# Performance work log

Measured on AMD Instinct MI355X. Metric: run time of the kernel, lower is better.

The kernel has to match this reference:

```python
import jax, jax.numpy as jnp
import numpy as np

B, Cin, H, W = 1024, 384, 14, 14
C = 768        # out_dim of stage (embed_dim[-1])
HEADS = 24
WIN = 7        # window clamped to post-merge resolution (7x7), shift=0
HID = 512      # cpb_mlp hidden width (timm SwinV2 default)
MLP = 4 * C


def _rel_tables(win):
    # log-spaced continuous relative coords table [ (2w-1)^2, 2 ]
    rng = np.arange(-(win - 1), win, dtype=np.float32)
    t = np.stack(np.meshgrid(rng, rng, indexing='ij'), axis=-1)
    t = t / (win - 1) * 8.0  # pretrained_window_size == 0 branch
    t = np.sign(t) * np.log2(np.abs(t) + 1.0) / np.log2(8.0)
    coords = np.stack(np.meshgrid(np.arange(win), np.arange(win), indexing='ij'))
    cf = coords.reshape(2, -1)
    rel = (cf[:, :, None] - cf[:, None, :]).transpose(1, 2, 0).astype(np.int64)
    rel[:, :, 0] += win - 1
    rel[:, :, 1] += win - 1
    rel[:, :, 0] *= 2 * win - 1
    idx = rel.sum(-1)
    return jnp.asarray(t.reshape(-1, 2)), jnp.asarray(idx.reshape(-1))


def _ln(x, g, b, eps=1e-5):
    mu = jnp.mean(x, axis=-1, keepdims=True)
    var = jnp.mean(jnp.square(x - mu), axis=-1, keepdims=True)
    return (x - mu) * jax.lax.rsqrt(var + eps) * g + b


def setup_inputs() -> dict:
    key = jax.random.key(0)
    ks = jax.random.split(key, 8)
    s = 0.02
    return dict(
        x=jax.random.normal(ks[0], (B, Cin, H, W), jnp.float32),
        merge_w=jax.random.normal(ks[1], (C, 4 * Cin), jnp.float32) * s,
        merge_gamma=jnp.ones((C,), jnp.float32),
        merge_beta=jnp.zeros((C,), jnp.float32),
        qkv_w=jax.random.normal(ks[2], (2, 3 * C, C), jnp.float32) * s,
        q_bias=jnp.zeros((2, C), jnp.float32),
        v_bias=jnp.zeros((2, C), jnp.float32),
        logit_scale=jnp.full((2, HEADS, 1, 1), float(np.log(10.0)), jnp.float32),
        cpb_w1=jax.random.normal(ks[3], (2, HID, 2), jnp.float32) * s,
        cpb_b1=jnp.zeros((2, HID), jnp.float32),
        cpb_w2=jax.random.normal(ks[4], (2, HEADS, HID), jnp.float32) * s,
        proj_w=jax.random.normal(ks[5], (2, C, C), jnp.float32) * s,
        proj_b=jnp.zeros((2, C), jnp.float32),
        n1_g=jnp.ones((2, C), jnp.float32),
        n1_b=jnp.zeros((2, C), jnp.float32),
        fc1_w=jax.random.normal(ks[6], (2, MLP, C), jnp.float32) * s,
        fc1_b=jnp.zeros((2, MLP), jnp.float32),
        fc2_w=jax.random.normal(ks[7], (2, C, MLP), jnp.float32) * s,
        fc2_b=jnp.zeros((2, C), jnp.float32),
        n2_g=jnp.ones((2, C), jnp.float32),
        n2_b=jnp.zeros((2, C), jnp.float32),
    )


def reference(x, merge_w, merge_gamma, merge_beta, qkv_w, q_bias, v_bias,
              logit_scale, cpb_w1, cpb_b1, cpb_w2, proj_w, proj_b, n1_g, n1_b,
              fc1_w, fc1_b, fc2_w, fc2_b, n2_g, n2_b):
    table, idx = _rel_tables(WIN)
    hd = C // HEADS
    N = WIN * WIN
    # NCHW -> NHWC
    h = jnp.transpose(x, (0, 2, 3, 1))
    Bn = h.shape[0]
    # PatchMerging (SwinV2: reduction then norm)
    h = h.reshape(Bn, H // 2, 2, W // 2, 2, Cin).transpose(0, 1, 3, 4, 2, 5)
    h = h.reshape(Bn, H // 2, W // 2, 4 * Cin)
    h = h @ merge_w.T
    h = _ln(h, merge_gamma, merge_beta)
    h = h.reshape(Bn, N, C)  # single 7x7 window per ROI, shift=0
    max_ls = jnp.log(jnp.asarray(100.0, h.dtype))  # clamp logit_scale at log(1/0.01)
    for i in range(2):  # two structurally-identical blocks (post-norm)
        bias_qkv = jnp.concatenate([q_bias[i], jnp.zeros_like(q_bias[i]), v_bias[i]])
        qkv = (h @ qkv_w[i].T + bias_qkv).reshape(Bn, N, 3, HEADS, hd)
        q, k, v = jnp.moveaxis(qkv, 2, 0)  # each [B, N, HEADS, hd]
        q = q / jnp.maximum(jnp.linalg.norm(q, axis=-1, keepdims=True), 1e-12)
        k = k / jnp.maximum(jnp.linalg.norm(k, axis=-1, keepdims=True), 1e-12)
        attn = jnp.einsum('bnhd,bmhd->bhnm', q, k)
        attn = attn * jnp.exp(jnp.minimum(logit_scale[i], max_ls))  # [HEADS,1,1]
        # continuous relative position bias
        cpb = jax.nn.relu(table @ cpb_w1[i].T + cpb_b1[i]) @ cpb_w2[i].T  # [(2w-1)^2, HEADS]
        rpb = cpb[idx].reshape(N, N, HEADS).transpose(2, 0, 1)
        attn = attn + 16.0 * jax.nn.sigmoid(rpb)
        attn = jax.nn.softmax(attn, axis=-1)
        out = jnp.einsum('bhnm,bmhd->bnhd', attn, v).reshape(Bn, N, C)
        out = out @ proj_w[i].T + proj_b[i]
        h = h + _ln(out, n1_g[i], n1_b[i])  # post-norm residual
        m = jax.nn.gelu(h @ fc1_w[i].T + fc1_b[i], approximate=False)
        m = m @ fc2_w[i].T + fc2_b[i]
        h = h + _ln(m, n2_g[i], n2_b[i])
    h = h.reshape(Bn, WIN, WIN, C)
    return jnp.transpose(h, (0, 3, 1, 2))  # NHWC -> NCHW
```

## Files before the change

### kernel.cpp

```cpp
#include <hip/hip_runtime.h>

typedef unsigned short u16;
typedef unsigned int u32;
typedef __bf16 bf16x8 __attribute__((ext_vector_type(8)));
typedef float f32x4 __attribute__((ext_vector_type(4)));

#define AS1 __attribute__((address_space(1)))
#define AS3 __attribute__((address_space(3)))

__device__ __forceinline__ float b2f(u16 u) {
    u32 x = ((u32)u) << 16; float f; __builtin_memcpy(&f, &x, 4); return f;
}
__device__ __forceinline__ u16 f2b(float f) {
    u32 x; __builtin_memcpy(&x, &f, 4);
    x += 0x7fffu + ((x >> 16) & 1u);
    return (u16)(x >> 16);
}
__device__ __forceinline__ void gload16(void* s, const void* g) {
    __builtin_amdgcn_global_load_lds((const AS1 void*)g, (AS3 void*)s, 16, 0, 0);
}

__global__ void detect_kernel(const u32* __restrict__ mg, u32* __restrict__ flag) {
    if (threadIdx.x == 0) *flag = (mg[0] == 0x3F803F80u) ? 1u : 0u;
}

struct CvtW { const void* src[5]; long off[5]; int n[5]; };
__global__ __launch_bounds__(256) void cvt_w_kernel(CvtW J, u16* __restrict__ wbase,
                                                    const u32* __restrict__ flag) {
    const int tId = blockIdx.y;
    const long i0 = (long)blockIdx.x * 2048 + threadIdx.x * 8;
    if (i0 >= J.n[tId]) return;
    u16* dst = wbase + J.off[tId] + i0;
    if (*flag) {
        *(uint4*)dst = *((const uint4*)((const u16*)J.src[tId] + i0));
    } else {
        const float* s = (const float*)J.src[tId] + i0;
        u32 w[4];
#pragma unroll
        for (int k = 0; k < 4; k++)
            w[k] = (u32)f2b(s[2 * k]) | ((u32)f2b(s[2 * k + 1]) << 16);
        *(uint4*)dst = make_uint4(w[0], w[1], w[2], w[3]);
    }
}

struct CvtP { const void* src[15]; long off[15]; int n[15]; };
__global__ __launch_bounds__(256) void cvt_p_kernel(CvtP J, float* __restrict__ pbase,
                                                    const u32* __restrict__ flag) {
    const int tId = blockIdx.y;
    const long i0 = (long)blockIdx.x * 2048 + threadIdx.x * 8;
    if (i0 >= J.n[tId]) return;
    float* dst = pbase + J.off[tId] + i0;
    if (*flag) {
        const u16* s = (const u16*)J.src[tId] + i0;
#pragma unroll
        for (int k = 0; k < 8; k++) dst[k] = b2f(s[k]);
    } else {
        const float* s = (const float*)J.src[tId] + i0;
        *(float4*)dst = *(const float4*)s;
        *(float4*)(dst + 4) = *(const float4*)(s + 4);
    }
}

__global__ __launch_bounds__(256) void gather_merge(const void* __restrict__ xv,
                                                    u16* __restrict__ Am,
                                                    const u32* __restrict__ flag) {
    __shared__ __align__(16) char sraw[64 * 196 * 4];
    const int b = blockIdx.x, cc = blockIdx.y;
    const int t = threadIdx.x;
    const int isbf = *flag;
    if (isbf) {
        const u16* xp = (const u16*)xv + ((long)b * 384 + cc * 64) * 196;
        for (int i = t; i < 1568; i += 256)
            ((uint4*)sraw)[i] = ((const uint4*)xp)[i];
    } else {
        const float* xp = (const float*)xv + ((long)b * 384 + cc * 64) * 196;
        for (int i = t; i < 3136; i += 256)
            ((uint4*)sraw)[i] = ((const uint4*)xp)[i];
    }
    __syncthreads();
    const int c = t & 63, q = t >> 6;
    for (int sg = q; sg < 196; sg += 4) {
        const int sidx = sg >> 2, g = sg & 3;
        const int h2 = sidx / 7, w2 = sidx % 7, hi = g & 1, wi = g >> 1;
        const int hw = (2 * h2 + hi) * 14 + (2 * w2 + wi);
        const u16 val = isbf ? ((const u16*)sraw)[c * 196 + hw]
                             : f2b(((const float*)sraw)[c * 196 + hw]);
        Am[((long)b * 49 + sidx) * 1536 + g * 384 + cc * 64 + c] = val;
    }
}

template <int EPI>
__global__ __launch_bounds__(256) void gemm_bt(const u16* __restrict__ A,
                                               const u16* __restrict__ W,
                                               const float* __restrict__ bias,
                                               u16* __restrict__ D,
                                               int M, int N, int K) {
    __shared__ __align__(16) u16 sA[128 * 32];
    __shared__ __align__(16) u16 sB[128 * 32];
    const int t = threadIdx.x;
    const int lane = t & 63;
    const int wave = t >> 6;
    const long rowA0 = (long)blockIdx.y * 128;
    const long rowB0 = (long)blockIdx.x * 128;
    const int wm = (wave >> 1) * 64;
    const int wn = (wave & 1) * 64;

    f32x4 acc[4][4];
#pragma unroll
    for (int i = 0; i < 4; i++)
#pragma unroll
        for (int j = 0; j < 4; j++) acc[i][j] = (f32x4){0.f, 0.f, 0.f, 0.f};

    const int srow = t >> 2;
    const int scol = (t & 3) * 8;
    const int fr = lane & 15;
    const int fk = (lane >> 4) * 8;

    const u16* Ag = A + rowA0 * K;
    const u16* Bg = W + rowB0 * K;
    char* sAb = (char*)sA;
    char* sBb = (char*)sB;
    const int wb = wave * 1024;

    for (int kk = 0; kk < K; kk += 32) {
        gload16(sAb + wb,        Ag + (long)srow * K + kk + scol);
        gload16(sAb + 4096 + wb, Ag + (long)(64 + srow) * K + kk + scol);
        gload16(sBb + wb,        Bg + (long)srow * K + kk + scol);
        gload16(sBb + 4096 + wb, Bg + (long)(64 + srow) * K + kk + scol);
        __syncthreads();
        bf16x8 af[4], bf[4];
#pragma unroll
        for (int mt = 0; mt < 4; mt++)
            af[mt] = *(const bf16x8*)&sA[(wm + mt * 16 + fr) * 32 + fk];
#pragma unroll
        for (int nt = 0; nt < 4; nt++)
            bf[nt] = *(const bf16x8*)&sB[(wn + nt * 16 + fr) * 32 + fk];
#pragma unroll
        for (int mt = 0; mt < 4; mt++)
#pragma unroll
            for (int nt = 0; nt < 4; nt++)
                acc[mt][nt] = __builtin_amdgcn_mfma_f32_16x16x32_bf16(
                    af[mt], bf[nt], acc[mt][nt], 0, 0, 0);
        __syncthreads();
    }

#pragma unroll
    for (int mt = 0; mt < 4; mt++) {
#pragma unroll
        for (int nt = 0; nt < 4; nt++) {
            const long col = rowB0 + wn + nt * 16 + (lane & 15);
            const float bv = bias ? bias[col] : 0.f;
#pragma unroll
            for (int r = 0; r < 4; r++) {
                const long row = rowA0 + wm + mt * 16 + (lane >> 4) * 4 + r;
                float v = acc[mt][nt][r] + bv;
                if (EPI == 1) v = 0.5f * v * (1.f + erff(v * 0.70710678118654752f));
                D[row * N + col] = f2b(v);
            }
        }
    }
}

__global__ __launch_bounds__(256) void ln_kernel(const u16* __restrict__ y,
                                                 const float* __restrict__ gw,
                                                 const float* __restrict__ bw,
                                                 float* __restrict__ h32,
                                                 u16* __restrict__ hb, int add) {
    const int row = blockIdx.x * 4 + (threadIdx.x >> 6);
    const int lane = threadIdx.x & 63;
    const u16* yr = y + (long)row * 768;
    float v[12];
    float s = 0.f, s2 = 0.f;
#pragma unroll
    for (int c = 0; c < 3; c++) {
        uint2 u = *(const uint2*)(yr + c * 256 + lane * 4);
        u16 p[4]; __builtin_memcpy(p, &u, 8);
#pragma unroll
        for (int e = 0; e < 4; e++) {
            float f = b2f(p[e]); v[c * 4 + e] = f; s += f; s2 += f * f;
        }
    }
#pragma unroll
    for (int off = 32; off > 0; off >>= 1) {
        s += __shfl_down(s, off); s2 += __shfl_down(s2, off);
    }
    s = __shfl(s, 0); s2 = __shfl(s2, 0);
    const float mu = s * (1.f / 768.f);
    const float var = s2 * (1.f / 768.f) - mu * mu;
    const float rs = rsqrtf(fmaxf(var, 0.f) + 1e-5f);
#pragma unroll
    for (int c = 0; c < 3; c++) {
        const int idx = c * 256 + lane * 4;
        const float4 g4 = *(const float4*)(gw + idx);
        const float4 b4 = *(const float4*)(bw + idx);
        float o[4];
        o[0] = (v[c * 4 + 0] - mu) * rs * g4.x + b4.x;
        o[1] = (v[c * 4 + 1] - mu) * rs * g4.y + b4.y;
        o[2] = (v[c * 4 + 2] - mu) * rs * g4.z + b4.z;
        o[3] = (v[c * 4 + 3] - mu) * rs * g4.w + b4.w;
        const long gi = (long)row * 768 + idx;
        if (add) {
            float4 h4 = *(float4*)&h32[gi];
            o[0] += h4.x; o[1] += h4.y; o[2] += h4.z; o[3] += h4.w;
        }
        *(float4*)&h32[gi] = make_float4(o[0], o[1], o[2], o[3]);
        uint2 pk;
        pk.x = (u32)f2b(o[0]) | ((u32)f2b(o[1]) << 16);
        pk.y = (u32)f2b(o[2]) | ((u32)f2b(o[3]) << 16);
        *(uint2*)&hb[gi] = pk;
    }
}

__device__ __forceinline__ float reltab(int i) {
    float r = (float)(i - 6) * (8.f / 6.f);
    float a = fabsf(r);
    return copysignf(log2f(a + 1.f) * (1.f / 3.f), r);
}
__global__ __launch_bounds__(256) void cpb_kernel(const float* __restrict__ w1,
                                                  const float* __restrict__ b1,
                                                  const float* __restrict__ w2,
                                                  float* __restrict__ cpb) {
    __shared__ float hid[512];
    const int e = blockIdx.x;
    const float t0 = reltab(e / 13), t1 = reltab(e % 13);
    for (int k = threadIdx.x; k < 512; k += 256)
        hid[k] = fmaxf(w1[2 * k] * t0 + w1[2 * k + 1] * t1 + b1[k], 0.f);
    __syncthreads();
    const int wave = threadIdx.x >> 6, lane = threadIdx.x & 63;
    for (int h = wave; h < 24; h += 4) {
        float sum = 0.f;
        for (int k = lane; k < 512; k += 64) sum += w2[h * 512 + k] * hid[k];
#pragma unroll
        for (int off = 32; off > 0; off >>= 1) sum += __shfl_down(sum, off);
        if (lane == 0) cpb[e * 24 + h] = sum;
    }
}

__global__ void bias16_kernel(const float* __restrict__ cpb,
                              float* __restrict__ b16) {
    const int tid = blockIdx.x * 256 + threadIdx.x;
    if (tid >= 24 * 2401) return;
    const int h = tid / 2401, nm = tid % 2401;
    const int n = nm / 49, m = nm % 49;
    const int e = (n / 7 - m / 7 + 6) * 13 + (n % 7 - m % 7 + 6);
    b16[tid] = 16.f / (1.f + expf(-cpb[e * 24 + h]));
}

__global__ void qkvbias_kernel(const float* __restrict__ qb,
                               const float* __restrict__ vb,
                               float* __restrict__ out) {
    const int j = blockIdx.x * 256 + threadIdx.x;
    if (j >= 2304) return;
    float v = 0.f;
    if (j < 768) v = qb[j];
    else if (j >= 1536) v = vb[j - 1536];
    out[j] = v;
}

#define APAIRS 4
__global__ __launch_bounds__(256) void attn_kernel(const u16* __restrict__ qkv,
                                                   const float* __restrict__ b16,
                                                   const float* __restrict__ ls,
                                                   u16* __restrict__ out) {
    __shared__ float sk[APAIRS][49 * 33 + 3];
    __shared__ float sv[APAIRS][49 * 32];
    __shared__ float rk[APAIRS][52];
    const int wave = threadIdx.x >> 6;
    const int lane = threadIdx.x & 63;
    const int head = blockIdx.x;
    const int b = blockIdx.y * APAIRS + wave;
    const long base = (long)b * 49 * 2304 + head * 32;
    float* skw = sk[wave];
    float* svw = sv[wave];

    for (int qi = lane; qi < 392; qi += 64) {
        const int m = qi >> 3, d0 = (qi & 7) * 4;
        const long r = base + (long)m * 2304 + d0;
        uint2 kk = *(const uint2*)(qkv + r + 768);
        uint2 vv = *(const uint2*)(qkv + r + 1536);
        u16 kp[4], vp[4];
        __builtin_memcpy(kp, &kk, 8);
        __builtin_memcpy(vp, &vv, 8);
        const int ko = m * 33 + d0;
        const int vo = m * 32 + d0;
#pragma unroll
        for (int e = 0; e < 4; e++) {
            skw[ko + e] = b2f(kp[e]);
            svw[vo + e] = b2f(vp[e]);
        }
    }
    __syncthreads();
    const int n = lane;
    if (n < 49) {
        float ss = 0.f;
#pragma unroll
        for (int d = 0; d < 32; d++) { float kv = skw[n * 33 + d]; ss += kv * kv; }
        rk[wave][n] = 1.f / fmaxf(sqrtf(ss), 1e-12f);
    }
    __syncthreads();
    if (n >= 49) return;

    float q[32]; float ss = 0.f;
    {
        const u16* qp = qkv + base + (long)n * 2304;
#pragma unroll
        for (int c = 0; c < 4; c++) {
            uint4 u = *(const uint4*)(qp + c * 8);
            u16 p[8]; __builtin_memcpy(p, &u, 16);
#pragma unroll
            for (int e = 0; e < 8; e++) {
                float f = b2f(p[e]); q[c * 8 + e] = f; ss += f * f;
            }
        }
    }
    const float rq = 1.f / fmaxf(sqrtf(ss), 1e-12f);
    const float cs = expf(fminf(ls[head], 4.6051701859880914f)) * rq;
    const float* bb = b16 + head * 2401 + n * 49;
    const float* rkw = rk[wave];
    float sarr[49], mx = -1e30f;
#pragma unroll
    for (int m = 0; m < 49; m++) {
        float dot = 0.f;
#pragma unroll
        for (int d = 0; d < 32; d++) dot += q[d] * skw[m * 33 + d];
        float val = dot * cs * rkw[m] + bb[m];
        sarr[m] = val; mx = fmaxf(mx, val);
    }
    float sum = 0.f;
#pragma unroll
    for (int m = 0; m < 49; m++) { sarr[m] = __expf(sarr[m] - mx); sum += sarr[m]; }
    const float rsum = 1.f / sum;
    float o[32];
#pragma unroll
    for (int d = 0; d < 32; d++) o[d] = 0.f;
#pragma unroll
    for (int m = 0; m < 49; m++) {
        const float p = sarr[m];
        const float* vr = svw + m * 32;
#pragma unroll
        for (int d = 0; d < 32; d++) o[d] += p * vr[d];
    }
    u16* op = out + ((long)b * 49 + n) * 768 + head * 32;
#pragma unroll
    for (int d = 0; d < 32; d += 2) {
        u32 pk = (u32)f2b(o[d] * rsum) | ((u32)f2b(o[d + 1] * rsum) << 16);
        *(u32*)&op[d] = pk;
    }
}

__global__ __launch_bounds__(256) void out_transpose(const float* __restrict__ h32,
                                                     void* __restrict__ outv,
                                                     const u32* __restrict__ flag) {
    __shared__ __align__(16) float sbuf[49 * 196];
    const int b = blockIdx.x, cc = blockIdx.y;
    const float* hp = h32 + (long)b * 49 * 768 + cc * 192;
    for (int i = threadIdx.x; i < 49 * 48; i += 256) {
        const int r = i / 48, v = i % 48;
        *(float4*)&sbuf[r * 196 + v * 4] = *(const float4*)&hp[(long)r * 768 + v * 4];
    }
    __syncthreads();
    const int isbf = *flag;
    if (isbf) {
        u16* out = (u16*)outv;
        for (int i = threadIdx.x; i < 192 * 49; i += 256) {
            const int c = i / 49, s = i % 49;
            out[((long)b * 768 + cc * 192 + c) * 49 + s] = f2b(sbuf[s * 196 + c]);
        }
    } else {
        float* out = (float*)outv;
        for (int i = threadIdx.x; i < 192 * 49; i += 256) {
            const int c = i / 49, s = i % 49;
            out[((long)b * 768 + cc * 192 + c) * 49 + s] = sbuf[s * 196 + c];
        }
    }
}

extern "C" void kernel_launch(void* const* d_in, const int* in_sizes, int n_in,
                              void* d_out, int out_size, void* d_ws, size_t ws_size,
                              hipStream_t stream) {
    char* ws = (char*)d_ws;
    float* h32  = (float*)(ws + 0L);
    u16*   hb   = (u16*)  (ws + 154140672L);
    u16*   ybuf = (u16*)  (ws + 231211008L);
    u16*   attn = (u16*)  (ws + 308281344L);
    u16*   big  = (u16*)  (ws + 385351680L);
    u16*   wbuf = (u16*)  (ws + 693633024L);
    float* prm  = (float*)(ws + 724303872L);
    float* cpb  = (float*)(ws + 724494528L);
    float* b16  = (float*)(ws + 724510752L);
    float* qkvb = (float*)(ws + 724741248L);
    u32*   flag = (u32*)  (ws + 724750464L);

    const int M = 50176;

    detect_kernel<<<1, 64, 0, stream>>>((const u32*)d_in[2], flag);

    CvtW jw;
    jw.src[0] = d_in[1];  jw.off[0] = 0;        jw.n[0] = 1179648;
    jw.src[1] = d_in[4];  jw.off[1] = 1179648;  jw.n[1] = 3538944;
    jw.src[2] = d_in[11]; jw.off[2] = 4718592;  jw.n[2] = 1179648;
    jw.src[3] = d_in[15]; jw.off[3] = 5898240;  jw.n[3] = 4718592;
    jw.src[4] = d_in[17]; jw.off[4] = 10616832; jw.n[4] = 4718592;
    cvt_w_kernel<<<dim3(2304, 5), 256, 0, stream>>>(jw, wbuf, flag);

    static const int pidx[15] = {2, 3, 5, 6, 7, 8, 9, 10, 12, 13, 14, 16, 18, 19, 20};
    static const int pn[15]   = {768, 768, 1536, 1536, 48, 2048, 1024, 24576,
                                 1536, 1536, 1536, 6144, 1536, 1536, 1536};
    CvtP jp; long po = 0; long poff[15];
    for (int i = 0; i < 15; i++) {
        jp.src[i] = d_in[pidx[i]]; jp.off[i] = po; jp.n[i] = pn[i];
        poff[i] = po; po += pn[i];
    }
    cvt_p_kernel<<<dim3(12, 15), 256, 0, stream>>>(jp, prm, flag);
    const float* p_merge_g = prm + poff[0];
    const float* p_merge_b = prm + poff[1];
    const float* p_qb      = prm + poff[2];
    const float* p_vb      = prm + poff[3];
    const float* p_ls      = prm + poff[4];
    const float* p_cw1     = prm + poff[5];
    const float* p_cb1     = prm + poff[6];
    const float* p_cw2     = prm + poff[7];
    const float* p_projb   = prm + poff[8];
    const float* p_n1g     = prm + poff[9];
    const float* p_n1b     = prm + poff[10];
    const float* p_fc1b    = prm + poff[11];
    const float* p_fc2b    = prm + poff[12];
    const float* p_n2g     = prm + poff[13];
    const float* p_n2b     = prm + poff[14];

    const u16* w_merge = wbuf;
    const u16* w_qkv   = wbuf + 1179648;
    const u16* w_proj  = wbuf + 4718592;
    const u16* w_fc1   = wbuf + 5898240;
    const u16* w_fc2   = wbuf + 10616832;

    gather_merge<<<dim3(1024, 6), 256, 0, stream>>>(d_in[0], big, flag);
    gemm_bt<0><<<dim3(6, 392), 256, 0, stream>>>(big, w_merge, nullptr, ybuf, M, 768, 1536);
    ln_kernel<<<12544, 256, 0, stream>>>(ybuf, p_merge_g, p_merge_b, h32, hb, 0);

    for (int i = 0; i < 2; i++) {
        qkvbias_kernel<<<9, 256, 0, stream>>>(p_qb + i * 768, p_vb + i * 768, qkvb);
        cpb_kernel<<<169, 256, 0, stream>>>(p_cw1 + i * 1024, p_cb1 + i * 512,
                                            p_cw2 + i * 12288, cpb);
        bias16_kernel<<<226, 256, 0, stream>>>(cpb, b16);
        gemm_bt<0><<<dim3(18, 392), 256, 0, stream>>>(hb, w_qkv + (long)i * 2304 * 768,
                                                      qkvb, big, M, 2304, 768);
        attn_kernel<<<dim3(24, 256), 256, 0, stream>>>(big, b16, p_ls + i * 24, attn);
        gemm_bt<0><<<dim3(6, 392), 256, 0, stream>>>(attn, w_proj + (long)i * 768 * 768,
                                                     p_projb + i * 768, ybuf, M, 768, 768);
        ln_kernel<<<12544, 256, 0, stream>>>(ybuf, p_n1g + i * 768, p_n1b + i * 768, h32, hb, 1);
        gemm_bt<1><<<dim3(24, 392), 256, 0, stream>>>(hb, w_fc1 + (long)i * 3072 * 768,
                                                      p_fc1b + i * 3072, big, M, 3072, 768);
        gemm_bt<0><<<dim3(6, 392), 256, 0, stream>>>(big, w_fc2 + (long)i * 768 * 3072,
                                                     p_fc2b + i * 768, ybuf, M, 768, 3072);
        ln_kernel<<<12544, 256, 0, stream>>>(ybuf, p_n2g + i * 768, p_n2b + i * 768, h32, hb, 1);
    }

    out_transpose<<<dim3(1024, 4), 256, 0, stream>>>(h32, d_out, flag);
}
```

Baseline: 4.346 ms.

## Rewrite GEMM as 256x256 triple-buffered pipelined kernel with swizzled LDS

Replaces the 128x128 single-stage bf16 GEMM with a 256x256 tile, 512-thread kernel. It triple-buffers LDS with global-to-LDS prefetch two k-steps ahead, XOR-swizzles the LDS layout to avoid bank conflicts, and interleaves MFMA bursts with loads under setprio and barriers. It also remaps workgroups across the XCDs for locality and replaces erff in the GELU epilogue with a polynomial approximation. The goal is to hide memory latency and raise MFMA utilisation, at the cost of higher register and LDS use and a slightly less accurate GELU.

```diff
diff --git a/kernel.cpp b/kernel.cpp
--- a/kernel.cpp
+++ b/kernel.cpp
@@ -18,6 +18,16 @@
 }
 __device__ __forceinline__ void gload16(void* s, const void* g) {
     __builtin_amdgcn_global_load_lds((const AS1 void*)g, (AS3 void*)s, 16, 0, 0);
+}
+__device__ __forceinline__ float gelu_f(float v) {
+    const float x = v * 0.70710678118654752f;
+    const float ax = fabsf(x);
+    const float t = 1.f / (1.f + 0.3275911f * ax);
+    float poly = ((((1.061405429f * t - 1.453152027f) * t) + 1.421413741f) * t
+                  - 0.284496736f) * t + 0.254829592f;
+    float erfv = 1.f - poly * t * __expf(-x * x);
+    erfv = copysignf(erfv, x);
+    return 0.5f * v * (1.f + erfv);
 }
 
 __global__ void detect_kernel(const u32* __restrict__ mg, u32* __restrict__ flag) {
@@ -89,72 +99,125 @@
     }
 }
 
+__device__ __forceinline__ void stage_tile(u16* __restrict__ lds,
+                                           const u16* __restrict__ g,
+                                           int K, int kk, int w, int lane) {
+    const int cb = (lane & 3) ^ ((lane >> 2) & 3);
+#pragma unroll
+    for (int c = 0; c < 2; c++) {
+        const int r = w * 32 + c * 16 + (lane >> 2);
+        gload16(lds + (w * 32 + c * 16) * 32, g + (long)r * K + kk + cb * 8);
+    }
+}
+
 template <int EPI>
-__global__ __launch_bounds__(256) void gemm_bt(const u16* __restrict__ A,
-                                               const u16* __restrict__ W,
-                                               const float* __restrict__ bias,
-                                               u16* __restrict__ D,
-                                               int M, int N, int K) {
-    __shared__ __align__(16) u16 sA[128 * 32];
-    __shared__ __align__(16) u16 sB[128 * 32];
-    const int t = threadIdx.x;
-    const int lane = t & 63;
-    const int wave = t >> 6;
-    const long rowA0 = (long)blockIdx.y * 128;
-    const long rowB0 = (long)blockIdx.x * 128;
-    const int wm = (wave >> 1) * 64;
-    const int wn = (wave & 1) * 64;
-
-    f32x4 acc[4][4];
-#pragma unroll
-    for (int i = 0; i < 4; i++)
-#pragma unroll
-        for (int j = 0; j < 4; j++) acc[i][j] = (f32x4){0.f, 0.f, 0.f, 0.f};
-
-    const int srow = t >> 2;
-    const int scol = (t & 3) * 8;
-    const int fr = lane & 15;
-    const int fk = (lane >> 4) * 8;
-
+__global__ __launch_bounds__(512, 2) void gemm_bt(const u16* __restrict__ A,
+                                                  const u16* __restrict__ W,
+                                                  const float* __restrict__ bias,
+                                                  u16* __restrict__ D,
+                                                  int M, int N, int K) {
+    __shared__ __align__(16) u16 sA[3][256 * 32];
+    __shared__ __align__(16) u16 sB[3][256 * 32];
+    const int tid = threadIdx.x;
+    const int lane = tid & 63;
+    const int w = tid >> 6;
+    const int wr = w >> 2;
+    const int wc = w & 3;
+
+    const int gN = gridDim.x, gM = gridDim.y;
+    const int nwg = gN * gM;
+    const int orig = blockIdx.y * gN + blockIdx.x;
+    const int q = nwg >> 3, rr = nwg & 7;
+    const int xcd = orig & 7, idx = orig >> 3;
+    const int wg = (xcd < rr ? xcd * (q + 1) : rr * (q + 1) + (xcd - rr) * q) + idx;
+    const int tn = wg / gM, tm = wg % gM;
+    const long rowA0 = (long)tm * 256;
+    const long rowB0 = (long)tn * 256;
     const u16* Ag = A + rowA0 * K;
     const u16* Bg = W + rowB0 * K;
-    char* sAb = (char*)sA;
-    char* sBb = (char*)sB;
-    const int wb = wave * 1024;
-
-    for (int kk = 0; kk < K; kk += 32) {
-        gload16(sAb + wb,        Ag + (long)srow * K + kk + scol);
-        gload16(sAb + 4096 + wb, Ag + (long)(64 + srow) * K + kk + scol);
-        gload16(sBb + wb,        Bg + (long)srow * K + kk + scol);
-        gload16(sBb + 4096 + wb, Bg + (long)(64 + srow) * K + kk + scol);
-        __syncthreads();
-        bf16x8 af[4], bf[4];
-#pragma unroll
-        for (int mt = 0; mt < 4; mt++)
-            af[mt] = *(const bf16x8*)&sA[(wm + mt * 16 + fr) * 32 + fk];
-#pragma unroll
-        for (int nt = 0; nt < 4; nt++)
-            bf[nt] = *(const bf16x8*)&sB[(wn + nt * 16 + fr) * 32 + fk];
-#pragma unroll
-        for (int mt = 0; mt < 4; mt++)
-#pragma unroll
-            for (int nt = 0; nt < 4; nt++)
-                acc[mt][nt] = __builtin_amdgcn_mfma_f32_16x16x32_bf16(
-                    af[mt], bf[nt], acc[mt][nt], 0, 0, 0);
-        __syncthreads();
-    }
-
-#pragma unroll
-    for (int mt = 0; mt < 4; mt++) {
-#pragma unroll
-        for (int nt = 0; nt < 4; nt++) {
-            const long col = rowB0 + wn + nt * 16 + (lane & 15);
+
+    f32x4 acc[8][4];
+#pragma unroll
+    for (int i = 0; i < 8; i++)
+#pragma unroll
+        for (int j = 0; j < 4; j++) acc[i][j] = (f32x4){0.f, 0.f, 0.f, 0.f};
+
+    const int fr = lane & 15;
+    const int rhi = lane >> 4;
+    const int kosw8 = ((lane >> 4) ^ (lane & 3)) * 8;
+
+    const int nt = K >> 5;
+    stage_tile(sA[0], Ag, K, 0, w, lane);
+    stage_tile(sB[0], Bg, K, 0, w, lane);
+    stage_tile(sA[1], Ag, K, 32, w, lane);
+    stage_tile(sB[1], Bg, K, 32, w, lane);
+    asm volatile("s_waitcnt vmcnt(4)" ::: "memory");
+    __builtin_amdgcn_s_barrier();
+
+    int cur = 0;
+    for (int t = 0; t < nt; t++) {
+        const u16* cA = sA[cur];
+        const u16* cB = sB[cur];
+        const int nb = (cur == 0) ? 2 : cur - 1;
+        const bool st = (t + 2) < nt;
+        bf16x8 bfr[4], afr[4];
+#pragma unroll
+        for (int j = 0; j < 4; j++) {
+            const int rB = wc * 64 + j * 16 + fr;
+            bfr[j] = *(const bf16x8*)&cB[rB * 32 + kosw8];
+        }
+#pragma unroll
+        for (int m = 0; m < 4; m++) {
+            const int rA = wr * 128 + m * 16 + fr;
+            afr[m] = *(const bf16x8*)&cA[rA * 32 + kosw8];
+        }
+        if (st) stage_tile(sA[nb], Ag, K, (t + 2) * 32, w, lane);
+        __builtin_amdgcn_s_barrier();
+        asm volatile("s_waitcnt lgkmcnt(0)" ::: "memory");
+        __builtin_amdgcn_sched_barrier(0);
+        __builtin_amdgcn_s_setprio(1);
+#pragma unroll
+        for (int m = 0; m < 4; m++)
+#pragma unroll
+            for (int j = 0; j < 4; j++)
+                acc[m][j] = __builtin_amdgcn_mfma_f32_16x16x32_bf16(
+                    afr[m], bfr[j], acc[m][j], 0, 0, 0);
+        __builtin_amdgcn_s_setprio(0);
+        __builtin_amdgcn_s_barrier();
+#pragma unroll
+        for (int m = 0; m < 4; m++) {
+            const int rA = wr * 128 + (m + 4) * 16 + fr;
+            afr[m] = *(const bf16x8*)&cA[rA * 32 + kosw8];
+        }
+        if (st) stage_tile(sB[nb], Bg, K, (t + 2) * 32, w, lane);
+        __builtin_amdgcn_s_barrier();
+        asm volatile("s_waitcnt lgkmcnt(0)" ::: "memory");
+        __builtin_amdgcn_sched_barrier(0);
+        __builtin_amdgcn_s_setprio(1);
+#pragma unroll
+        for (int m = 0; m < 4; m++)
+#pragma unroll
+            for (int j = 0; j < 4; j++)
+                acc[m + 4][j] = __builtin_amdgcn_mfma_f32_16x16x32_bf16(
+                    afr[m], bfr[j], acc[m + 4][j], 0, 0, 0);
+        __builtin_amdgcn_s_setprio(0);
+        if (st) { asm volatile("s_waitcnt vmcnt(4)" ::: "memory"); }
+        else    { asm volatile("s_waitcnt vmcnt(0)" ::: "memory"); }
+        __builtin_amdgcn_s_barrier();
+        cur = (cur == 2) ? 0 : cur + 1;
+    }
+
+#pragma unroll
+    for (int m = 0; m < 8; m++) {
+#pragma unroll
+        for (int j = 0; j < 4; j++) {
+            const long col = rowB0 + wc * 64 + j * 16 + fr;
             const float bv = bias ? bias[col] : 0.f;
 #pragma unroll
             for (int r = 0; r < 4; r++) {
-                const long row = rowA0 + wm + mt * 16 + (lane >> 4) * 4 + r;
-                float v = acc[mt][nt][r] + bv;
-                if (EPI == 1) v = 0.5f * v * (1.f + erff(v * 0.70710678118654752f));
+                const long row = rowA0 + wr * 128 + m * 16 + rhi * 4 + r;
+                float v = acc[m][j][r] + bv;
+                if (EPI == 1) v = gelu_f(v);
                 D[row * N + col] = f2b(v);
             }
         }
@@ -435,7 +498,7 @@
     const u16* w_fc2   = wbuf + 10616832;
 
     gather_merge<<<dim3(1024, 6), 256, 0, stream>>>(d_in[0], big, flag);
-    gemm_bt<0><<<dim3(6, 392), 256, 0, stream>>>(big, w_merge, nullptr, ybuf, M, 768, 1536);
+    gemm_bt<0><<<dim3(3, 196), 512, 0, stream>>>(big, w_merge, nullptr, ybuf, M, 768, 1536);
     ln_kernel<<<12544, 256, 0, stream>>>(ybuf, p_merge_g, p_merge_b, h32, hb, 0);
 
     for (int i = 0; i < 2; i++) {
@@ -443,15 +506,15 @@
         cpb_kernel<<<169, 256, 0, stream>>>(p_cw1 + i * 1024, p_cb1 + i * 512,
                                             p_cw2 + i * 12288, cpb);
         bias16_kernel<<<226, 256, 0, stream>>>(cpb, b16);
-        gemm_bt<0><<<dim3(18, 392), 256, 0, stream>>>(hb, w_qkv + (long)i * 2304 * 768,
-                                                      qkvb, big, M, 2304, 768);
+        gemm_bt<0><<<dim3(9, 196), 512, 0, stream>>>(hb, w_qkv + (long)i * 2304 * 768,
+                                                     qkvb, big, M, 2304, 768);
         attn_kernel<<<dim3(24, 256), 256, 0, stream>>>(big, b16, p_ls + i * 24, attn);
-        gemm_bt<0><<<dim3(6, 392), 256, 0, stream>>>(attn, w_proj + (long)i * 768 * 768,
+        gemm_bt<0><<<dim3(3, 196), 512, 0, stream>>>(attn, w_proj + (long)i * 768 * 768,
                                                      p_projb + i * 768, ybuf, M, 768, 768);
         ln_kernel<<<12544, 256, 0, stream>>>(ybuf, p_n1g + i * 768, p_n1b + i * 768, h32, hb, 1);
-        gemm_bt<1><<<dim3(24, 392), 256, 0, stream>>>(hb, w_fc1 + (long)i * 3072 * 768,
+        gemm_bt<1><<<dim3(12, 196), 512, 0, stream>>>(hb, w_fc1 + (long)i * 3072 * 768,
                                                       p_fc1b + i * 3072, big, M, 3072, 768);
-        gemm_bt<0><<<dim3(6, 392), 256, 0, stream>>>(big, w_fc2 + (long)i * 768 * 3072,
+        gemm_bt<0><<<dim3(3, 196), 512, 0, stream>>>(big, w_fc2 + (long)i * 768 * 3072,
                                                      p_fc2b + i * 768, ybuf, M, 768, 3072);
         ln_kernel<<<12544, 256, 0, stream>>>(ybuf, p_n2g + i * 768, p_n2b + i * 768, h32, hb, 1);
     }
```

Measured after the change: 3.983 ms. 8.3% less time.
